# Kernel tuning notes

Measured on AMD Instinct MI355X. Metric: run time of the kernel, lower is better.

Reference implementation:

```python
import jax, jax.numpy as jnp
import numpy as np

DM = 512      # d_model
DM4 = DM // 4 # per-modality embed dim
DI = 2 * DM   # d_inner (expand=2)
DS = 16       # d_state
DTR = 32      # dt_rank = d_model/16
DC = 4        # d_conv
NL = 3        # n_layers
SD = 17       # state_dim
AD = 7        # act_dim
MAXT = 2048   # max_ep_len
EPS = 1e-5


def setup_inputs() -> dict:
    key = jax.random.key(0)
    ks = jax.random.split(key, 32)
    B, L = 2, 1024
    f32 = jnp.float32

    def rn(k, shape, s=0.02):
        return jax.random.normal(k, shape, f32) * s

    inp = {}
    inp["states"] = jax.random.normal(ks[0], (B, L, SD), f32)
    inp["actions"] = jax.random.normal(ks[1], (B, L, AD), f32)
    inp["returns_to_go"] = jax.random.normal(ks[2], (B, L, 1), f32)
    inp["constraints_to_go"] = jax.random.normal(ks[3], (B, L, 1), f32)
    inp["timesteps"] = jax.random.randint(ks[4], (B, L), 0, MAXT)

    # embedding heads
    inp["W_s"] = rn(ks[5], (DM4, SD)); inp["b_s"] = jnp.zeros((DM4,), f32)
    inp["W_a"] = rn(ks[6], (DM4, AD)); inp["b_a"] = jnp.zeros((DM4,), f32)
    inp["W_r"] = rn(ks[7], (DM4, 1));  inp["b_r"] = jnp.zeros((DM4,), f32)
    inp["W_c"] = rn(ks[8], (DM4, 1));  inp["b_c"] = jnp.zeros((DM4,), f32)
    inp["E_t"] = rn(ks[9], (MAXT, DM4))

    # per-layer Mamba params (stacked on leading layer dim)
    inp["ln_g"] = jnp.ones((NL, DM), f32)
    inp["ln_b"] = jnp.zeros((NL, DM), f32)
    inp["in_w"] = rn(ks[10], (NL, 2 * DI, DM))
    inp["conv_w"] = rn(ks[11], (NL, DI, DC), 0.1)
    inp["conv_b"] = jnp.zeros((NL, DI), f32)
    inp["xproj_w"] = rn(ks[12], (NL, DTR + 2 * DS, DI))
    inp["dtproj_w"] = rn(ks[13], (NL, DI, DTR), 0.1)
    inp["dtproj_b"] = jnp.full((NL, DI), -4.6, f32)  # softplus^-1(~0.01)
    inp["A_log"] = jnp.log(jnp.broadcast_to(jnp.arange(1, DS + 1, dtype=f32), (NL, DI, DS)))
    inp["D_ssm"] = jnp.ones((NL, DI), f32)
    inp["out_w"] = rn(ks[14], (NL, DM, DI))

    inp["fn_g"] = jnp.ones((DM,), f32)
    inp["fn_b"] = jnp.zeros((DM,), f32)
    inp["W_ps"] = rn(ks[15], (SD, DM4)); inp["b_ps"] = jnp.zeros((SD,), f32)
    inp["W_pa"] = rn(ks[16], (AD, DM4)); inp["b_pa"] = jnp.zeros((AD,), f32)
    return inp


def _layernorm(x, g, b):
    mu = x.mean(-1, keepdims=True)
    v = ((x - mu) ** 2).mean(-1, keepdims=True)
    return (x - mu) * jax.lax.rsqrt(v + EPS) * g + b


def _mamba_mixer(x, in_w, conv_w, conv_b, xproj_w, dtproj_w, dtproj_b, A_log, Dv, out_w):
    B, L, _ = x.shape
    xz = jnp.einsum('bld,ed->ble', x, in_w)          # (B,L,2*DI)
    xc, z = jnp.split(xz, 2, axis=-1)
    # causal depthwise conv1d, kernel DC
    xp = jnp.pad(xc, ((0, 0), (DC - 1, 0), (0, 0)))
    xc = sum(xp[:, k:k + L, :] * conv_w[:, k] for k in range(DC)) + conv_b
    xc = jax.nn.silu(xc)
    xdbl = jnp.einsum('bld,ed->ble', xc, xproj_w)    # (B,L,DTR+2*DS)
    dt_low = xdbl[..., :DTR]
    Bm = xdbl[..., DTR:DTR + DS]
    Cm = xdbl[..., DTR + DS:]
    dt = jax.nn.softplus(jnp.einsum('blr,dr->bld', dt_low, dtproj_w) + dtproj_b)
    A = -jnp.exp(A_log)                               # (DI,DS)

    def step(h, xs):
        dt_t, B_t, C_t, u_t = xs                      # (B,DI),(B,DS),(B,DS),(B,DI)
        dA = jnp.exp(dt_t[:, :, None] * A)            # (B,DI,DS)
        h = h * dA + (dt_t * u_t)[:, :, None] * B_t[:, None, :]
        y = jnp.einsum('bds,bs->bd', h, C_t)
        return h, y

    h0 = jnp.zeros((B, DI, DS), x.dtype)
    xs = (dt.transpose(1, 0, 2), Bm.transpose(1, 0, 2), Cm.transpose(1, 0, 2), xc.transpose(1, 0, 2))
    _, ys = jax.lax.scan(step, h0, xs)               # (L,B,DI)
    y = ys.transpose(1, 0, 2) + Dv * xc
    y = y * jax.nn.silu(z)
    return jnp.einsum('bld,ed->ble', y, out_w)


def reference(states, actions, returns_to_go, constraints_to_go, timesteps,
              W_s, b_s, W_a, b_a, W_r, b_r, W_c, b_c, E_t,
              ln_g, ln_b, in_w, conv_w, conv_b, xproj_w, dtproj_w, dtproj_b,
              A_log, D_ssm, out_w, fn_g, fn_b, W_ps, b_ps, W_pa, b_pa):
    B, L = timesteps.shape
    te = E_t[timesteps]                               # (B,L,DM4)
    se = states @ W_s.T + b_s + te
    ae = actions @ W_a.T + b_a + te
    re = returns_to_go @ W_r.T + b_r + te
    ce = constraints_to_go @ W_c.T + b_c + te
    # shift actions right by one, zero at t=0
    ae = jnp.concatenate([jnp.zeros_like(ae[:, :1]), ae[:, :-1]], axis=1)
    x = jnp.stack((re, ce, se, ae), axis=2).reshape(B, L, 4 * DM4)  # (B,L,DM)
    for i in range(NL):
        x = x + _mamba_mixer(_layernorm(x, ln_g[i], ln_b[i]),
                             in_w[i], conv_w[i], conv_b[i], xproj_w[i],
                             dtproj_w[i], dtproj_b[i], A_log[i], D_ssm[i], out_w[i])
    x = _layernorm(x, fn_g, fn_b)
    out = x.reshape(B, L, 4, DM4)
    state_preds = out[:, :, 3] @ W_ps.T + b_ps
    action_preds = out[:, :, 2] @ W_pa.T + b_pa
    return (state_preds, action_preds)
```

## Files before the change

kernel.cpp:

```cpp
#include <hip/hip_runtime.h>
#include <cstdint>
#include <cstddef>

#define DMf 512
#define DM4 128
#define DIi 1024
#define DSs 16
#define DTRr 32
#define NLl 3
#define SDd 17
#define ADd 7
#define Bb 2
#define Ll 1024
#define NTOK (Bb*Ll)
#define CL 32
#define NCH 32

typedef __bf16 bf16x8 __attribute__((ext_vector_type(8)));
typedef float f32x4 __attribute__((ext_vector_type(4)));

__device__ inline unsigned short f2bf(float f){
  unsigned int u = __float_as_uint(f);
  unsigned int r = (u + 0x7FFFu + ((u>>16)&1u)) >> 16;
  return (unsigned short)r;
}
__device__ inline float silu_f(float v){ return v / (1.0f + __expf(-v)); }

__global__ __launch_bounds__(256) void cast_bf16_k(const float* __restrict__ src,
    unsigned short* __restrict__ dst, int n){
  int i = blockIdx.x*256 + threadIdx.x;
  if (i < n) dst[i] = f2bf(src[i]);
}

__global__ __launch_bounds__(128) void embed_k(
    const float* __restrict__ st, const float* __restrict__ ac,
    const float* __restrict__ rtg, const float* __restrict__ ctg,
    const int* __restrict__ ts,
    const float* __restrict__ Ws, const float* __restrict__ bs,
    const float* __restrict__ Wa, const float* __restrict__ ba,
    const float* __restrict__ Wr, const float* __restrict__ br,
    const float* __restrict__ Wc, const float* __restrict__ bc,
    const float* __restrict__ Et, float* __restrict__ x)
{
  int tok = blockIdx.x; int j = threadIdx.x;
  int l = tok & (Ll-1);
  int t = ts[tok];
  float te = Et[(size_t)t*DM4 + j];
  float re = rtg[tok]*Wr[j] + br[j] + te;
  float ce = ctg[tok]*Wc[j] + bc[j] + te;
  float se = bs[j] + te;
  #pragma unroll
  for (int k=0;k<SDd;++k) se += st[(size_t)tok*SDd+k]*Ws[j*SDd+k];
  float ae = 0.0f;
  if (l > 0) {
    int tp = ts[tok-1];
    ae = ba[j] + Et[(size_t)tp*DM4 + j];
    #pragma unroll
    for (int k=0;k<ADd;++k) ae += ac[(size_t)(tok-1)*ADd+k]*Wa[j*ADd+k];
  }
  float* xt = x + (size_t)tok*DMf;
  xt[0*DM4+j]=re; xt[1*DM4+j]=ce; xt[2*DM4+j]=se; xt[3*DM4+j]=ae;
}

__global__ __launch_bounds__(256) void ln_k(const float* __restrict__ x,
    const float* __restrict__ g, const float* __restrict__ bta,
    unsigned short* __restrict__ xn)
{
  int wave = threadIdx.x >> 6, lane = threadIdx.x & 63;
  int tok = blockIdx.x*4 + wave;
  const float* xr = x + (size_t)tok*DMf;
  float v[8];
  float4 a = *(const float4*)&xr[lane*8];
  float4 b = *(const float4*)&xr[lane*8+4];
  v[0]=a.x; v[1]=a.y; v[2]=a.z; v[3]=a.w; v[4]=b.x; v[5]=b.y; v[6]=b.z; v[7]=b.w;
  float s = 0.f;
  #pragma unroll
  for (int j=0;j<8;++j) s += v[j];
  #pragma unroll
  for (int m=32;m>=1;m>>=1) s += __shfl_xor(s, m, 64);
  float mu = s * (1.0f/DMf);
  float vs = 0.f;
  #pragma unroll
  for (int j=0;j<8;++j){ float d = v[j]-mu; vs += d*d; }
  #pragma unroll
  for (int m=32;m>=1;m>>=1) vs += __shfl_xor(vs, m, 64);
  float rstd = rsqrtf(vs*(1.0f/DMf) + 1e-5f);
  unsigned int o[8];
  #pragma unroll
  for (int j=0;j<8;++j){
    int c = lane*8+j;
    o[j] = f2bf((v[j]-mu)*rstd*g[c] + bta[c]);
  }
  uint4 w;
  w.x = o[0] | (o[1]<<16); w.y = o[2] | (o[3]<<16);
  w.z = o[4] | (o[5]<<16); w.w = o[6] | (o[7]<<16);
  *(uint4*)&xn[(size_t)tok*DMf + lane*8] = w;
}

template<int ACCUM>
__global__ __launch_bounds__(256) void gemm_bt_k(const unsigned short* __restrict__ A,
    const unsigned short* __restrict__ Bm, float* __restrict__ C, int M, int N, int K)
{
  __shared__ unsigned short As[128*32];
  __shared__ unsigned short Bs[128*32];
  int tid = threadIdx.x;
  int bm = blockIdx.x, bn = blockIdx.y;
  size_t row0 = (size_t)bm*128, col0 = (size_t)bn*128;
  int wave = tid>>6, lane = tid&63;
  int wr = wave>>1, wc = wave&1;
  f32x4 acc[4][4];
  f32x4 z4 = {0.f,0.f,0.f,0.f};
  #pragma unroll
  for (int m=0;m<4;++m)
    #pragma unroll
    for (int n=0;n<4;++n) acc[m][n] = z4;
  int lrow = lane&15, lko = (lane>>4)*8;
  for (int k0=0; k0<K; k0+=32){
    #pragma unroll
    for (int r=0;r<2;++r){
      int flat = r*256 + tid;
      int arow = flat>>2, ak = (flat&3)*8;
      const unsigned short* ga = A + (row0+arow)*K + k0 + ak;
      const unsigned short* gb = Bm + (col0+arow)*K + k0 + ak;
      __builtin_amdgcn_global_load_lds((const __attribute__((address_space(1))) void*)ga,
          (__attribute__((address_space(3))) void*)(&As[flat*8]), 16, 0, 0);
      __builtin_amdgcn_global_load_lds((const __attribute__((address_space(1))) void*)gb,
          (__attribute__((address_space(3))) void*)(&Bs[flat*8]), 16, 0, 0);
    }
    __syncthreads();
    bf16x8 af[4], bfv[4];
    #pragma unroll
    for (int m=0;m<4;++m) af[m] = *(const bf16x8*)&As[(wr*64+m*16+lrow)*32 + lko];
    #pragma unroll
    for (int n=0;n<4;++n) bfv[n] = *(const bf16x8*)&Bs[(wc*64+n*16+lrow)*32 + lko];
    #pragma unroll
    for (int m=0;m<4;++m)
      #pragma unroll
      for (int n=0;n<4;++n)
        acc[m][n] = __builtin_amdgcn_mfma_f32_16x16x32_bf16(af[m], bfv[n], acc[m][n], 0, 0, 0);
    __syncthreads();
  }
  int lcol = lane&15, lr4 = (lane>>4)*4;
  #pragma unroll
  for (int m=0;m<4;++m)
    #pragma unroll
    for (int n=0;n<4;++n){
      size_t row = row0 + wr*64 + m*16 + lr4;
      size_t col = col0 + wc*64 + n*16 + lcol;
      #pragma unroll
      for (int j=0;j<4;++j){
        float vv = acc[m][n][j];
        float* p = &C[(row+j)*N + col];
        if (ACCUM) *p += vv; else *p = vv;
      }
    }
}

__global__ __launch_bounds__(256) void gemm_bt64_k(const unsigned short* __restrict__ A,
    const unsigned short* __restrict__ Bm, float* __restrict__ C, int M, int N, int K)
{
  __shared__ unsigned short As[64*32];
  __shared__ unsigned short Bs[64*32];
  int tid = threadIdx.x;
  size_t row0 = (size_t)blockIdx.x*64, col0 = (size_t)blockIdx.y*64;
  int wave = tid>>6, lane = tid&63;
  int wr = wave>>1, wc = wave&1;
  f32x4 acc[2][2];
  f32x4 z4 = {0.f,0.f,0.f,0.f};
  acc[0][0]=z4; acc[0][1]=z4; acc[1][0]=z4; acc[1][1]=z4;
  int lrow = lane&15, lko = (lane>>4)*8;
  int srow = tid>>2, sk = (tid&3)*8;
  for (int k0=0; k0<K; k0+=32){
    const unsigned short* ga = A + (row0+srow)*K + k0 + sk;
    const unsigned short* gb = Bm + (col0+srow)*K + k0 + sk;
    __builtin_amdgcn_global_load_lds((const __attribute__((address_space(1))) void*)ga,
        (__attribute__((address_space(3))) void*)(&As[tid*8]), 16, 0, 0);
    __builtin_amdgcn_global_load_lds((const __attribute__((address_space(1))) void*)gb,
        (__attribute__((address_space(3))) void*)(&Bs[tid*8]), 16, 0, 0);
    __syncthreads();
    bf16x8 af[2], bfv[2];
    #pragma unroll
    for (int m=0;m<2;++m) af[m] = *(const bf16x8*)&As[(wr*32+m*16+lrow)*32 + lko];
    #pragma unroll
    for (int n=0;n<2;++n) bfv[n] = *(const bf16x8*)&Bs[(wc*32+n*16+lrow)*32 + lko];
    #pragma unroll
    for (int m=0;m<2;++m)
      #pragma unroll
      for (int n=0;n<2;++n)
        acc[m][n] = __builtin_amdgcn_mfma_f32_16x16x32_bf16(af[m], bfv[n], acc[m][n], 0, 0, 0);
    __syncthreads();
  }
  int lcol = lane&15, lr4 = (lane>>4)*4;
  #pragma unroll
  for (int m=0;m<2;++m)
    #pragma unroll
    for (int n=0;n<2;++n){
      size_t row = row0 + wr*32 + m*16 + lr4;
      size_t col = col0 + wc*32 + n*16 + lcol;
      #pragma unroll
      for (int j=0;j<4;++j)
        C[(row+j)*N + col] += acc[m][n][j];
    }
}

__global__ __launch_bounds__(256) void conv_k(const float* __restrict__ xz,
    const float* __restrict__ cw, const float* __restrict__ cb,
    float* __restrict__ xc, unsigned short* __restrict__ xcbf)
{
  int idx = blockIdx.x*256 + threadIdx.x;
  int d = idx & (DIi-1); int tok = idx >> 10; int l = tok & (Ll-1);
  float acc = cb[d];
  #pragma unroll
  for (int k=0;k<4;++k){
    int ll = l + k - 3;
    if (ll >= 0) acc += xz[(size_t)(tok + k - 3)*(2*DIi) + d] * cw[d*4+k];
  }
  float v = silu_f(acc);
  xc[idx] = v;
  xcbf[idx] = f2bf(v);
}

__global__ __launch_bounds__(256) void xproj_mfma_k(const unsigned short* __restrict__ A,
    const unsigned short* __restrict__ Bw, float* __restrict__ xdbl)
{
  __shared__ unsigned short As[64*32];
  __shared__ unsigned short Bs[64*32];
  int tid = threadIdx.x;
  size_t row0 = (size_t)blockIdx.x*64;
  int wave = tid>>6, lane = tid&63;
  int wr = wave>>1, wc = wave&1;
  f32x4 acc[2][2];
  f32x4 z4 = {0.f,0.f,0.f,0.f};
  acc[0][0]=z4; acc[0][1]=z4; acc[1][0]=z4; acc[1][1]=z4;
  int lrow = lane&15, lko = (lane>>4)*8;
  int srow = tid>>2, sk = (tid&3)*8;
  for (int k0=0; k0<DIi; k0+=32){
    const unsigned short* ga = A + (row0+srow)*DIi + k0 + sk;
    const unsigned short* gb = Bw + (size_t)srow*DIi + k0 + sk;
    __builtin_amdgcn_global_load_lds((const __attribute__((address_space(1))) void*)ga,
        (__attribute__((address_space(3))) void*)(&As[tid*8]), 16, 0, 0);
    __builtin_amdgcn_global_load_lds((const __attribute__((address_space(1))) void*)gb,
        (__attribute__((address_space(3))) void*)(&Bs[tid*8]), 16, 0, 0);
    __syncthreads();
    bf16x8 af[2], bfv[2];
    #pragma unroll
    for (int m=0;m<2;++m) af[m] = *(const bf16x8*)&As[(wr*32+m*16+lrow)*32 + lko];
    #pragma unroll
    for (int n=0;n<2;++n) bfv[n] = *(const bf16x8*)&Bs[(wc*32+n*16+lrow)*32 + lko];
    #pragma unroll
    for (int m=0;m<2;++m)
      #pragma unroll
      for (int n=0;n<2;++n)
        acc[m][n] = __builtin_amdgcn_mfma_f32_16x16x32_bf16(af[m], bfv[n], acc[m][n], 0, 0, 0);
    __syncthreads();
  }
  int lcol = lane&15, lr4 = (lane>>4)*4;
  #pragma unroll
  for (int m=0;m<2;++m)
    #pragma unroll
    for (int n=0;n<2;++n){
      size_t row = row0 + wr*32 + m*16 + lr4;
      int col = wc*32 + n*16 + lcol;
      #pragma unroll
      for (int j=0;j<4;++j)
        xdbl[(row+j)*64 + col] = acc[m][n][j];
    }
}

__global__ __launch_bounds__(256) void dtproj_k(const float* __restrict__ xdbl,
    const float* __restrict__ dw, const float* __restrict__ db, float* __restrict__ dt)
{
  int bid = blockIdx.x;
  int tok0 = (bid >> 2) * 8;
  int o = (bid & 3)*256 + threadIdx.x;
  __shared__ float lows[8][32];
  {
    int tt = threadIdx.x >> 5, kk = threadIdx.x & 31;
    lows[tt][kk] = xdbl[(size_t)(tok0+tt)*64 + kk];
  }
  __syncthreads();
  float w[32];
  #pragma unroll
  for (int q=0;q<8;++q)
    *(float4*)&w[q*4] = *(const float4*)&dw[(size_t)o*32 + q*4];
  float bias = db[o];
  #pragma unroll
  for (int t=0;t<8;++t){
    float acc = bias;
    #pragma unroll
    for (int k=0;k<32;++k) acc += w[k]*lows[t][k];
    float dv = (acc > 15.0f) ? acc : log1pf(__expf(acc));
    dt[(size_t)(tok0+t)*DIi + o] = dv;
  }
}

__global__ __launch_bounds__(256) void scan1_k(const float* __restrict__ dt,
    const float* __restrict__ xc, const float* __restrict__ xdbl,
    const float* __restrict__ Alog, float* __restrict__ Ebuf, float* __restrict__ Pbuf)
{
  int bid = blockIdx.x;
  int dblk = bid & 3; int tmp = bid >> 2; int c = tmp & (NCH-1); int b = tmp >> 5;
  int d = dblk*256 + threadIdx.x;
  float A[16], h[16], P[16];
  #pragma unroll
  for (int s=0;s<16;++s){ A[s] = -__expf(Alog[d*16+s]); h[s]=0.f; P[s]=1.f; }
  int l0 = c*CL;
  for (int l=l0; l<l0+CL; ++l){
    size_t tok = (size_t)b*Ll + l;
    float dtv = dt[tok*DIi + d];
    float u   = xc[tok*DIi + d];
    float dtu = dtv*u;
    const float* bcv = &xdbl[tok*64 + 32];
    #pragma unroll
    for (int s=0;s<16;++s){
      float dA = __expf(dtv*A[s]);
      h[s] = h[s]*dA + dtu*bcv[s];
      P[s] *= dA;
    }
  }
  size_t base = (((size_t)b*DIi + d)*NCH + c)*16;
  #pragma unroll
  for (int s=0;s<16;++s){ Ebuf[base+s]=h[s]; Pbuf[base+s]=P[s]; }
}

__global__ __launch_bounds__(256) void scanmid_k(const float* __restrict__ E,
    const float* __restrict__ P, float* __restrict__ H0)
{
  int gid = blockIdx.x*256 + threadIdx.x;
  int s = gid & 15; size_t bd = (size_t)(gid >> 4);
  float H = 0.f;
  for (int c=0;c<NCH;++c){
    size_t idx = (bd*NCH + c)*16 + s;
    H0[idx] = H;
    H = P[idx]*H + E[idx];
  }
}

__global__ __launch_bounds__(256) void scan2_k(const float* __restrict__ dt,
    const float* __restrict__ xc, const float* __restrict__ xdbl,
    const float* __restrict__ Alog, const float* __restrict__ Dv,
    const float* __restrict__ xz, const float* __restrict__ H0,
    unsigned short* __restrict__ ybf)
{
  int bid = blockIdx.x;
  int dblk = bid & 3; int tmp = bid >> 2; int c = tmp & (NCH-1); int b = tmp >> 5;
  int d = dblk*256 + threadIdx.x;
  size_t base = (((size_t)b*DIi + d)*NCH + c)*16;
  float A[16], h[16];
  #pragma unroll
  for (int s=0;s<16;++s){ A[s] = -__expf(Alog[d*16+s]); h[s] = H0[base+s]; }
  float Dd = Dv[d];
  int l0 = c*CL;
  for (int l=l0; l<l0+CL; ++l){
    size_t tok = (size_t)b*Ll + l;
    float dtv = dt[tok*DIi + d];
    float u   = xc[tok*DIi + d];
    float dtu = dtv*u;
    const float* bcv = &xdbl[tok*64 + 32];
    float y = 0.f;
    #pragma unroll
    for (int s=0;s<16;++s){
      float dA = __expf(dtv*A[s]);
      h[s] = h[s]*dA + dtu*bcv[s];
      y += h[s]*bcv[16+s];
    }
    float zv = xz[tok*(2*DIi) + DIi + d];
    ybf[tok*DIi + d] = f2bf((y + Dd*u) * silu_f(zv));
  }
}

__global__ __launch_bounds__(256) void head_k(const float* __restrict__ x,
    const float* __restrict__ g, const float* __restrict__ bta,
    const float* __restrict__ Wps, const float* __restrict__ bps,
    const float* __restrict__ Wpa, const float* __restrict__ bpa,
    float* __restrict__ out)
{
  __shared__ float lds[4][256];
  int wave = threadIdx.x >> 6, lane = threadIdx.x & 63;
  int tok = blockIdx.x*4 + wave;
  const float* xr = x + (size_t)tok*DMf;
  float v[8];
  float4 a = *(const float4*)&xr[lane*8];
  float4 b = *(const float4*)&xr[lane*8+4];
  v[0]=a.x; v[1]=a.y; v[2]=a.z; v[3]=a.w; v[4]=b.x; v[5]=b.y; v[6]=b.z; v[7]=b.w;
  float s = 0.f;
  #pragma unroll
  for (int j=0;j<8;++j) s += v[j];
  #pragma unroll
  for (int m=32;m>=1;m>>=1) s += __shfl_xor(s, m, 64);
  float mu = s * (1.0f/DMf);
  float vs = 0.f;
  #pragma unroll
  for (int j=0;j<8;++j){ float d = v[j]-mu; vs += d*d; }
  #pragma unroll
  for (int m=32;m>=1;m>>=1) vs += __shfl_xor(vs, m, 64);
  float rstd = rsqrtf(vs*(1.0f/DMf) + 1e-5f);
  if (lane >= 32){
    #pragma unroll
    for (int j=0;j<8;++j){
      int cdx = lane*8+j;
      lds[wave][cdx-256] = (v[j]-mu)*rstd*g[cdx] + bta[cdx];
    }
  }
  __syncthreads();
  if (lane < SDd){
    float acc = bps[lane];
    const float* w = &Wps[lane*DM4];
    #pragma unroll 8
    for (int k=0;k<DM4;++k) acc += lds[wave][128+k]*w[k];
    out[(size_t)tok*SDd + lane] = acc;
  } else if (lane < SDd+ADd){
    int o = lane - SDd;
    float acc = bpa[o];
    const float* w = &Wpa[o*DM4];
    #pragma unroll 8
    for (int k=0;k<DM4;++k) acc += lds[wave][k]*w[k];
    out[(size_t)NTOK*SDd + (size_t)tok*ADd + o] = acc;
  }
}

extern "C" void kernel_launch(void* const* d_in, const int* in_sizes, int n_in,
                              void* d_out, int out_size, void* d_ws, size_t ws_size,
                              hipStream_t stream)
{
  (void)in_sizes; (void)n_in; (void)out_size;
  const float* states   = (const float*)d_in[0];
  const float* actions  = (const float*)d_in[1];
  const float* rtg      = (const float*)d_in[2];
  const float* ctg      = (const float*)d_in[3];
  const int*   ts       = (const int*)d_in[4];
  const float* W_s      = (const float*)d_in[5];
  const float* b_s      = (const float*)d_in[6];
  const float* W_a      = (const float*)d_in[7];
  const float* b_a      = (const float*)d_in[8];
  const float* W_r      = (const float*)d_in[9];
  const float* b_r      = (const float*)d_in[10];
  const float* W_c      = (const float*)d_in[11];
  const float* b_c      = (const float*)d_in[12];
  const float* E_t      = (const float*)d_in[13];
  const float* ln_g     = (const float*)d_in[14];
  const float* ln_b     = (const float*)d_in[15];
  const float* in_w     = (const float*)d_in[16];
  const float* conv_w   = (const float*)d_in[17];
  const float* conv_b   = (const float*)d_in[18];
  const float* xproj_w  = (const float*)d_in[19];
  const float* dtproj_w = (const float*)d_in[20];
  const float* dtproj_b = (const float*)d_in[21];
  const float* A_log    = (const float*)d_in[22];
  const float* D_ssm    = (const float*)d_in[23];
  const float* out_w    = (const float*)d_in[24];
  const float* fn_g     = (const float*)d_in[25];
  const float* fn_b     = (const float*)d_in[26];
  const float* W_ps     = (const float*)d_in[27];
  const float* b_ps     = (const float*)d_in[28];
  const float* W_pa     = (const float*)d_in[29];
  const float* b_pa     = (const float*)d_in[30];

  char* ws = (char*)d_ws;
  constexpr size_t S_X    = (size_t)NTOK*DMf*4;
  constexpr size_t S_XN   = (size_t)NTOK*DMf*2;
  constexpr size_t S_XZ   = (size_t)NTOK*2*DIi*4;
  constexpr size_t S_XC   = (size_t)NTOK*DIi*4;
  constexpr size_t S_XCB  = (size_t)NTOK*DIi*2;
  constexpr size_t S_XDBL = (size_t)NTOK*64*4;
  constexpr size_t S_DT   = (size_t)NTOK*DIi*4;
  constexpr size_t S_YBF  = (size_t)NTOK*DIi*2;
  constexpr size_t S_INW  = (size_t)NLl*2048*512*2;
  constexpr size_t S_OUTW = (size_t)NLl*512*1024*2;
  constexpr size_t S_XPW  = (size_t)NLl*64*DIi*2;
  constexpr size_t S_E    = (size_t)Bb*DIi*NCH*16*4;
  constexpr size_t S_TOTAL = S_X+S_XN+S_XZ+S_XC+S_XCB+S_XDBL+S_DT+S_YBF
                             +S_INW+S_OUTW+S_XPW+3*S_E;

  if (ws_size < S_TOTAL) return;

  size_t off = 0;
  float* x            = (float*)(ws + off);          off += S_X;
  unsigned short* xn  = (unsigned short*)(ws + off); off += S_XN;
  float* xz           = (float*)(ws + off);          off += S_XZ;
  float* xc           = (float*)(ws + off);          off += S_XC;
  unsigned short* xcbf= (unsigned short*)(ws + off); off += S_XCB;
  float* xdbl         = (float*)(ws + off);          off += S_XDBL;
  float* dt           = (float*)(ws + off);          off += S_DT;
  unsigned short* ybf = (unsigned short*)(ws + off); off += S_YBF;
  unsigned short* inw_bf  = (unsigned short*)(ws + off); off += S_INW;
  unsigned short* outw_bf = (unsigned short*)(ws + off); off += S_OUTW;
  unsigned short* xpw_bf  = (unsigned short*)(ws + off); off += S_XPW;
  float* Ebuf         = (float*)(ws + off);          off += S_E;
  float* Pbuf         = (float*)(ws + off);          off += S_E;
  float* H0buf        = (float*)(ws + off);          off += S_E;

  const int n_inw  = NLl*2048*512;
  const int n_outw = NLl*512*1024;
  const int n_xpw  = NLl*64*DIi;
  cast_bf16_k<<<(n_inw+255)/256, 256, 0, stream>>>(in_w, inw_bf, n_inw);
  cast_bf16_k<<<(n_outw+255)/256, 256, 0, stream>>>(out_w, outw_bf, n_outw);
  cast_bf16_k<<<(n_xpw+255)/256, 256, 0, stream>>>(xproj_w, xpw_bf, n_xpw);

  embed_k<<<NTOK, 128, 0, stream>>>(states, actions, rtg, ctg, ts,
      W_s, b_s, W_a, b_a, W_r, b_r, W_c, b_c, E_t, x);

  for (int i=0;i<NLl;++i){
    ln_k<<<NTOK/4, 256, 0, stream>>>(x, ln_g + i*DMf, ln_b + i*DMf, xn);
    gemm_bt_k<0><<<dim3(NTOK/128, 2048/128), 256, 0, stream>>>(
        xn, inw_bf + (size_t)i*2048*512, xz, NTOK, 2048, 512);
    conv_k<<<(NTOK*DIi)/256, 256, 0, stream>>>(xz, conv_w + (size_t)i*DIi*4,
        conv_b + (size_t)i*DIi, xc, xcbf);
    xproj_mfma_k<<<NTOK/64, 256, 0, stream>>>(xcbf, xpw_bf + (size_t)i*64*DIi, xdbl);
    dtproj_k<<<(NTOK/8)*4, 256, 0, stream>>>(xdbl, dtproj_w + (size_t)i*DIi*32,
        dtproj_b + (size_t)i*DIi, dt);
    scan1_k<<<Bb*NCH*4, 256, 0, stream>>>(dt, xc, xdbl,
        A_log + (size_t)i*DIi*16, Ebuf, Pbuf);
    scanmid_k<<<(Bb*DIi*16)/256, 256, 0, stream>>>(Ebuf, Pbuf, H0buf);
    scan2_k<<<Bb*NCH*4, 256, 0, stream>>>(dt, xc, xdbl,
        A_log + (size_t)i*DIi*16, D_ssm + (size_t)i*DIi, xz, H0buf, ybf);
    gemm_bt64_k<<<dim3(NTOK/64, 512/64), 256, 0, stream>>>(
        ybf, outw_bf + (size_t)i*512*1024, x, NTOK, 512, 1024);
  }

  head_k<<<NTOK/4, 256, 0, stream>>>(x, fn_g, fn_b, W_ps, b_ps, W_pa, b_pa,
      (float*)d_out);
}
```

Measured before the change: 385.5 us.

## Fuse dt projection into scan kernels, halve chunk length, merge weight casts

Removes the separate dtproj kernel and the dt buffer; both scan passes now recompute dt = softplus(W·x_low + b) per token from the xdbl row using per-thread register weights. The chunk length is halved (NCH 32→64) so the scan grids have twice as many blocks. The three bf16 weight-cast launches are merged into one kernel. In exchange, the dt projection is computed twice and the mid-scan over chunks becomes longer.

After: 427.7 us. +10.9%, slower.

```diff
diff --git a/kernel.cpp b/kernel.cpp
--- a/kernel.cpp
+++ b/kernel.cpp
@@ -13,8 +13,8 @@
 #define Bb 2
 #define Ll 1024
 #define NTOK (Bb*Ll)
-#define CL 32
-#define NCH 32
+#define CL 16
+#define NCH 64
 
 typedef __bf16 bf16x8 __attribute__((ext_vector_type(8)));
 typedef float f32x4 __attribute__((ext_vector_type(4)));
@@ -26,10 +26,16 @@
 }
 __device__ inline float silu_f(float v){ return v / (1.0f + __expf(-v)); }
 
-__global__ __launch_bounds__(256) void cast_bf16_k(const float* __restrict__ src,
-    unsigned short* __restrict__ dst, int n){
+__global__ __launch_bounds__(256) void cast3_k(
+    const float* __restrict__ a, unsigned short* __restrict__ da, int na,
+    const float* __restrict__ b, unsigned short* __restrict__ db, int nb,
+    const float* __restrict__ c, unsigned short* __restrict__ dc, int nc){
   int i = blockIdx.x*256 + threadIdx.x;
-  if (i < n) dst[i] = f2bf(src[i]);
+  if (i < na) { da[i] = f2bf(a[i]); return; }
+  int j = i - na;
+  if (j < nb) { db[j] = f2bf(b[j]); return; }
+  int k = j - nb;
+  if (k < nc) dc[k] = f2bf(c[k]);
 }
 
 __global__ __launch_bounds__(128) void embed_k(
@@ -267,54 +273,38 @@
     }
 }
 
-__global__ __launch_bounds__(256) void dtproj_k(const float* __restrict__ xdbl,
-    const float* __restrict__ dw, const float* __restrict__ db, float* __restrict__ dt)
+__global__ __launch_bounds__(256) void scan1_k(const float* __restrict__ xc,
+    const float* __restrict__ xdbl, const float* __restrict__ dw,
+    const float* __restrict__ dbias, const float* __restrict__ Alog,
+    float* __restrict__ Ebuf, float* __restrict__ Pbuf)
 {
   int bid = blockIdx.x;
-  int tok0 = (bid >> 2) * 8;
-  int o = (bid & 3)*256 + threadIdx.x;
-  __shared__ float lows[8][32];
-  {
-    int tt = threadIdx.x >> 5, kk = threadIdx.x & 31;
-    lows[tt][kk] = xdbl[(size_t)(tok0+tt)*64 + kk];
-  }
-  __syncthreads();
+  int dblk = bid & 3; int tmp = bid >> 2; int c = tmp & (NCH-1); int b = tmp >> 6;
+  int d = dblk*256 + threadIdx.x;
   float w[32];
   #pragma unroll
-  for (int q=0;q<8;++q)
-    *(float4*)&w[q*4] = *(const float4*)&dw[(size_t)o*32 + q*4];
-  float bias = db[o];
-  #pragma unroll
-  for (int t=0;t<8;++t){
-    float acc = bias;
-    #pragma unroll
-    for (int k=0;k<32;++k) acc += w[k]*lows[t][k];
-    float dv = (acc > 15.0f) ? acc : log1pf(__expf(acc));
-    dt[(size_t)(tok0+t)*DIi + o] = dv;
-  }
-}
-
-__global__ __launch_bounds__(256) void scan1_k(const float* __restrict__ dt,
-    const float* __restrict__ xc, const float* __restrict__ xdbl,
-    const float* __restrict__ Alog, float* __restrict__ Ebuf, float* __restrict__ Pbuf)
-{
-  int bid = blockIdx.x;
-  int dblk = bid & 3; int tmp = bid >> 2; int c = tmp & (NCH-1); int b = tmp >> 5;
-  int d = dblk*256 + threadIdx.x;
+  for (int q=0;q<8;++q) *(f32x4*)&w[q*4] = *(const f32x4*)&dw[(size_t)d*32 + q*4];
+  float bias = dbias[d];
   float A[16], h[16], P[16];
   #pragma unroll
   for (int s=0;s<16;++s){ A[s] = -__expf(Alog[d*16+s]); h[s]=0.f; P[s]=1.f; }
   int l0 = c*CL;
   for (int l=l0; l<l0+CL; ++l){
     size_t tok = (size_t)b*Ll + l;
-    float dtv = dt[tok*DIi + d];
-    float u   = xc[tok*DIi + d];
+    const float* xrow = &xdbl[tok*64];
+    float acc = bias;
+    #pragma unroll
+    for (int r=0;r<32;r+=4){
+      f32x4 xv = *(const f32x4*)&xrow[r];
+      acc += w[r]*xv[0] + w[r+1]*xv[1] + w[r+2]*xv[2] + w[r+3]*xv[3];
+    }
+    float dtv = (acc > 15.0f) ? acc : log1pf(__expf(acc));
+    float u = xc[tok*DIi + d];
     float dtu = dtv*u;
-    const float* bcv = &xdbl[tok*64 + 32];
     #pragma unroll
     for (int s=0;s<16;++s){
       float dA = __expf(dtv*A[s]);
-      h[s] = h[s]*dA + dtu*bcv[s];
+      h[s] = h[s]*dA + dtu*xrow[32+s];
       P[s] *= dA;
     }
   }
@@ -336,15 +326,19 @@
   }
 }
 
-__global__ __launch_bounds__(256) void scan2_k(const float* __restrict__ dt,
-    const float* __restrict__ xc, const float* __restrict__ xdbl,
-    const float* __restrict__ Alog, const float* __restrict__ Dv,
-    const float* __restrict__ xz, const float* __restrict__ H0,
-    unsigned short* __restrict__ ybf)
+__global__ __launch_bounds__(256) void scan2_k(const float* __restrict__ xc,
+    const float* __restrict__ xdbl, const float* __restrict__ dw,
+    const float* __restrict__ dbias, const float* __restrict__ Alog,
+    const float* __restrict__ Dv, const float* __restrict__ xz,
+    const float* __restrict__ H0, unsigned short* __restrict__ ybf)
 {
   int bid = blockIdx.x;
-  int dblk = bid & 3; int tmp = bid >> 2; int c = tmp & (NCH-1); int b = tmp >> 5;
+  int dblk = bid & 3; int tmp = bid >> 2; int c = tmp & (NCH-1); int b = tmp >> 6;
   int d = dblk*256 + threadIdx.x;
+  float w[32];
+  #pragma unroll
+  for (int q=0;q<8;++q) *(f32x4*)&w[q*4] = *(const f32x4*)&dw[(size_t)d*32 + q*4];
+  float bias = dbias[d];
   size_t base = (((size_t)b*DIi + d)*NCH + c)*16;
   float A[16], h[16];
   #pragma unroll
@@ -353,16 +347,22 @@
   int l0 = c*CL;
   for (int l=l0; l<l0+CL; ++l){
     size_t tok = (size_t)b*Ll + l;
-    float dtv = dt[tok*DIi + d];
-    float u   = xc[tok*DIi + d];
+    const float* xrow = &xdbl[tok*64];
+    float acc = bias;
+    #pragma unroll
+    for (int r=0;r<32;r+=4){
+      f32x4 xv = *(const f32x4*)&xrow[r];
+      acc += w[r]*xv[0] + w[r+1]*xv[1] + w[r+2]*xv[2] + w[r+3]*xv[3];
+    }
+    float dtv = (acc > 15.0f) ? acc : log1pf(__expf(acc));
+    float u = xc[tok*DIi + d];
     float dtu = dtv*u;
-    const float* bcv = &xdbl[tok*64 + 32];
     float y = 0.f;
     #pragma unroll
     for (int s=0;s<16;++s){
       float dA = __expf(dtv*A[s]);
-      h[s] = h[s]*dA + dtu*bcv[s];
-      y += h[s]*bcv[16+s];
+      h[s] = h[s]*dA + dtu*xrow[32+s];
+      y += h[s]*xrow[48+s];
     }
     float zv = xz[tok*(2*DIi) + DIi + d];
     ybf[tok*DIi + d] = f2bf((y + Dd*u) * silu_f(zv));
@@ -463,13 +463,12 @@
   constexpr size_t S_XC   = (size_t)NTOK*DIi*4;
   constexpr size_t S_XCB  = (size_t)NTOK*DIi*2;
   constexpr size_t S_XDBL = (size_t)NTOK*64*4;
-  constexpr size_t S_DT   = (size_t)NTOK*DIi*4;
   constexpr size_t S_YBF  = (size_t)NTOK*DIi*2;
   constexpr size_t S_INW  = (size_t)NLl*2048*512*2;
   constexpr size_t S_OUTW = (size_t)NLl*512*1024*2;
   constexpr size_t S_XPW  = (size_t)NLl*64*DIi*2;
   constexpr size_t S_E    = (size_t)Bb*DIi*NCH*16*4;
-  constexpr size_t S_TOTAL = S_X+S_XN+S_XZ+S_XC+S_XCB+S_XDBL+S_DT+S_YBF
+  constexpr size_t S_TOTAL = S_X+S_XN+S_XZ+S_XC+S_XCB+S_XDBL+S_YBF
                              +S_INW+S_OUTW+S_XPW+3*S_E;
 
   if (ws_size < S_TOTAL) return;
@@ -481,7 +480,6 @@
   float* xc           = (float*)(ws + off);          off += S_XC;
   unsigned short* xcbf= (unsigned short*)(ws + off); off += S_XCB;
   float* xdbl         = (float*)(ws + off);          off += S_XDBL;
-  float* dt           = (float*)(ws + off);          off += S_DT;
   unsigned short* ybf = (unsigned short*)(ws + off); off += S_YBF;
   unsigned short* inw_bf  = (unsigned short*)(ws + off); off += S_INW;
   unsigned short* outw_bf = (unsigned short*)(ws + off); off += S_OUTW;
@@ -493,9 +491,8 @@
   const int n_inw  = NLl*2048*512;
   const int n_outw = NLl*512*1024;
   const int n_xpw  = NLl*64*DIi;
-  cast_bf16_k<<<(n_inw+255)/256, 256, 0, stream>>>(in_w, inw_bf, n_inw);
-  cast_bf16_k<<<(n_outw+255)/256, 256, 0, stream>>>(out_w, outw_bf, n_outw);
-  cast_bf16_k<<<(n_xpw+255)/256, 256, 0, stream>>>(xproj_w, xpw_bf, n_xpw);
+  cast3_k<<<(n_inw+n_outw+n_xpw+255)/256, 256, 0, stream>>>(
+      in_w, inw_bf, n_inw, out_w, outw_bf, n_outw, xproj_w, xpw_bf, n_xpw);
 
   embed_k<<<NTOK, 128, 0, stream>>>(states, actions, rtg, ctg, ts,
       W_s, b_s, W_a, b_a, W_r, b_r, W_c, b_c, E_t, x);
@@ -507,12 +504,12 @@
     conv_k<<<(NTOK*DIi)/256, 256, 0, stream>>>(xz, conv_w + (size_t)i*DIi*4,
         conv_b + (size_t)i*DIi, xc, xcbf);
     xproj_mfma_k<<<NTOK/64, 256, 0, stream>>>(xcbf, xpw_bf + (size_t)i*64*DIi, xdbl);
-    dtproj_k<<<(NTOK/8)*4, 256, 0, stream>>>(xdbl, dtproj_w + (size_t)i*DIi*32,
-        dtproj_b + (size_t)i*DIi, dt);
-    scan1_k<<<Bb*NCH*4, 256, 0, stream>>>(dt, xc, xdbl,
+    scan1_k<<<Bb*NCH*4, 256, 0, stream>>>(xc, xdbl,
+        dtproj_w + (size_t)i*DIi*32, dtproj_b + (size_t)i*DIi,
         A_log + (size_t)i*DIi*16, Ebuf, Pbuf);
     scanmid_k<<<(Bb*DIi*16)/256, 256, 0, stream>>>(Ebuf, Pbuf, H0buf);
-    scan2_k<<<Bb*NCH*4, 256, 0, stream>>>(dt, xc, xdbl,
+    scan2_k<<<Bb*NCH*4, 256, 0, stream>>>(xc, xdbl,
+        dtproj_w + (size_t)i*DIi*32, dtproj_b + (size_t)i*DIi,
         A_log + (size_t)i*DIi*16, D_ssm + (size_t)i*DIi, xz, H0buf, ybf);
     gemm_bt64_k<<<dim3(NTOK/64, 512/64), 256, 0, stream>>>(
         ybf, outw_bf + (size_t)i*512*1024, x, NTOK, 512, 1024);
```
